# Optimization experiments

Measured on AMD Instinct MI355X. Metric: run time of the kernel, lower is better.

## Reference

```python
import jax, jax.numpy as jnp
import numpy as np

B = 2048
NUM_FIELDS = 32
EMBED = 64
P = NUM_FIELDS * (NUM_FIELDS - 1) // 2  # 496 field pairs

# Pair indices (i < j), identical to the row_idx/col_idx loops in __init__
_ROW, _COL = np.triu_indices(NUM_FIELDS, k=1)
ROW_IDX = jnp.asarray(_ROW, dtype=jnp.int32)
COL_IDX = jnp.asarray(_COL, dtype=jnp.int32)


def setup_inputs() -> dict:
    key = jax.random.key(0)
    k1, k2 = jax.random.split(key)
    emb_inputs = jax.random.normal(k1, (B, NUM_FIELDS, EMBED), dtype=jnp.float32)
    # kernel_type='mat' -> kernel shape (E, P, E), xavier_normal-like init
    fan_in = P * EMBED
    fan_out = EMBED
    std = float(np.sqrt(2.0 / (fan_in + fan_out)))
    kernel = jax.random.normal(k2, (EMBED, P, EMBED), dtype=jnp.float32) * std
    return {"emb_inputs": emb_inputs, "kernel": kernel}


def reference(emb_inputs, kernel):
    # Gather field pairs: p, q shape (B, P, E)
    p = emb_inputs[:, ROW_IDX]
    q = emb_inputs[:, COL_IDX]
    # torch named-tensor chain for kernel_type='mat':
    #   kp[b, h, n] = sum_e p[b, n, e] * kernel[h, n, e]
    #   out[b, n]   = sum_h kp[b, h, n] * q[b, n, h]
    # Fused: out[b, n] = sum_{e, h} p[b, n, e] * kernel[h, n, e] * q[b, n, h]
    return jnp.einsum('bne,hne,bnh->bn', p, kernel, q)
```

## Files before the change

### kernel.cpp

```cpp
#include <hip/hip_runtime.h>


#define B_TOT 2048
#define NF    32
#define EMB   64
#define NP    496
#define BT    32

typedef short bf16x8 __attribute__((ext_vector_type(8)));
typedef short bf16x4 __attribute__((ext_vector_type(4)));
typedef float f32x4  __attribute__((ext_vector_type(4)));

static __device__ inline unsigned f2bf(float f) {
    unsigned u = __builtin_bit_cast(unsigned, f);
    u += 0x7fffu + ((u >> 16) & 1u);
    return u >> 16;
}
static __device__ inline unsigned pack2(float lo, float hi) {
    return f2bf(lo) | (f2bf(hi) << 16);
}
static __device__ inline float bf2f(short s) {
    return __builtin_bit_cast(float, (unsigned)((unsigned short)s) << 16);
}

#define AS1 __attribute__((address_space(1)))
#define AS3 __attribute__((address_space(3)))

__device__ const unsigned char PAIR_T16[120] = {
    0x01,0x02,0x03,0x04,0x05,0x06,0x07,0x08,0x09,0x0A,0x0B,0x0C,0x0D,0x0E,0x0F,
    0x12,0x13,0x14,0x15,0x16,0x17,0x18,0x19,0x1A,0x1B,0x1C,0x1D,0x1E,0x1F,
    0x23,0x24,0x25,0x26,0x27,0x28,0x29,0x2A,0x2B,0x2C,0x2D,0x2E,0x2F,
    0x34,0x35,0x36,0x37,0x38,0x39,0x3A,0x3B,0x3C,0x3D,0x3E,0x3F,
    0x45,0x46,0x47,0x48,0x49,0x4A,0x4B,0x4C,0x4D,0x4E,0x4F,
    0x56,0x57,0x58,0x59,0x5A,0x5B,0x5C,0x5D,0x5E,0x5F,
    0x67,0x68,0x69,0x6A,0x6B,0x6C,0x6D,0x6E,0x6F,
    0x78,0x79,0x7A,0x7B,0x7C,0x7D,0x7E,0x7F,
    0x89,0x8A,0x8B,0x8C,0x8D,0x8E,0x8F,
    0x9A,0x9B,0x9C,0x9D,0x9E,0x9F,
    0xAB,0xAC,0xAD,0xAE,0xAF,
    0xBC,0xBD,0xBE,0xBF,
    0xCD,0xCE,0xCF,
    0xDE,0xDF,
    0xEF
};

__global__ __launch_bounds__(256) void prep(const float* __restrict__ kern,
                                            const float* __restrict__ emb,
                                            short* __restrict__ kb,
                                            short* __restrict__ ebf) {
    __shared__ short w[EMB * 72];
    if (blockIdx.x < NP) {
        const int n = blockIdx.x;
#pragma unroll
        for (int j = 0; j < 4; ++j) {
            const int idx = threadIdx.x + 256 * j;
            const int h = idx >> 4, e4 = idx & 15;
            const f32x4 v = *(const f32x4*)(kern + ((size_t)h * NP + n) * EMB + e4 * 4);
            uint2 u;
            u.x = pack2(v[0], v[1]);
            u.y = pack2(v[2], v[3]);
            *(uint2*)&w[h * 72 + e4 * 4] = u;
        }
        __syncthreads();
#pragma unroll
        for (int j = 0; j < 2; ++j) {
            const int u    = threadIdx.x + 256 * j;
            const int frag = u >> 6, l = u & 63;
            const int h  = (frag >> 1) * 16 + (l & 15);
            const int e0 = (frag & 1) * 32 + (l >> 4) * 8;
            const bf16x8 t = *(const bf16x8*)&w[h * 72 + e0];
            *(bf16x8*)(kb + (size_t)n * 4096 + u * 8) = t;
        }
    } else {
        const int t    = (blockIdx.x - NP) * 256 + threadIdx.x;
        const int cidx = t & 127;
        const int f    = (t >> 7) & 31;
        const int bt16 = t >> 12;
        const int bp = cidx >> 3, x = cidx & 7;
        const int ec = x ^ (bp & 7);
        const float* src = emb + (((size_t)(bt16 * 16 + bp) * NF + f) * EMB + ec * 8);
        const f32x4 a = *(const f32x4*)src;
        const f32x4 b = *(const f32x4*)(src + 4);
        uint4 u;
        u.x = pack2(a[0], a[1]); u.y = pack2(a[2], a[3]);
        u.z = pack2(b[0], b[1]); u.w = pack2(b[2], b[3]);
        *(uint4*)(ebf + (size_t)t * 8) = u;
    }
}

__global__ __launch_bounds__(512, 4) void opnl_main(
    const short* __restrict__ ebf,
    const short* __restrict__ kb,
    float* __restrict__ out)
{
    __shared__ short elds[16 * 2 * 1024];

    const int type = blockIdx.x >> 6;
    const int bt   = blockIdx.x & 63;
    const int b0   = bt * BT;

    int bLo, bHi, npr;
    switch (type) {
        case 0: case 1: bLo = 0;  bHi = 0;  npr = 60; break;
        case 2: case 3: bLo = 16; bHi = 16; npr = 60; break;
        case 4:         bLo = 0;  bHi = 8;  npr = 64; break;
        case 5:         bLo = 8;  bHi = 16; npr = 64; break;
        case 6:         bLo = 0;  bHi = 16; npr = 64; break;
        default:        bLo = 8;  bHi = 8;  npr = 64; break;
    }

    const int lane = threadIdx.x & 63;
    const int wid  = threadIdx.x >> 6;
    const int lo4  = lane & 15;
    const int hi4  = lane >> 4;

#pragma unroll
    for (int i = 0; i < 4; ++i) {
        const int s   = wid * 4 + i;
        const int lf  = s >> 1, sub = s & 1;
        const int gf  = lf + (lf < 8 ? bLo : bHi);
        const short* src = ebf + ((size_t)((bt * 2 + sub) * 32 + gf)) * 1024;
        __builtin_amdgcn_global_load_lds((const AS1 void*)(src + lane * 8),
                                         (AS3 void*)&elds[s * 1024], 16, 0, 0);
        __builtin_amdgcn_global_load_lds((const AS1 void*)(src + 512 + lane * 8),
                                         (AS3 void*)&elds[s * 1024 + 512], 16, 0, 0);
    }
    __syncthreads();

    auto pairK = [&](int k, int& lr, int& lc, int& nn) {
        int pr = wid + 8 * k;
        if (pr >= npr) pr -= npr;
        if (type < 4) {
            const int pig = __builtin_amdgcn_readfirstlane((type & 1) * 60 + pr);
            const int byt = PAIR_T16[pig];
            lr = byt >> 4; lc = byt & 15;
        } else {
            lr = pr >> 3; lc = 8 + (pr & 7);
        }
        const int R = lr + (lr < 8 ? bLo : bHi);
        const int C = lc + (lc < 8 ? bLo : bHi);
        nn = R * (63 - R) / 2 + (C - R - 1);
    };

    auto loadW = [&](bf16x8 (&wf)[4][2], int nn) {
        const bf16x8* wp = (const bf16x8*)(kb + (size_t)nn * 4096);
#pragma unroll
        for (int mh = 0; mh < 4; ++mh)
#pragma unroll
            for (int kc = 0; kc < 2; ++kc)
                wf[mh][kc] = wp[(mh * 2 + kc) * 64 + lane];
    };

    auto compute = [&](bf16x8 (&wf)[4][2], int lr, int lc, int nn) {
#pragma unroll
        for (int sub = 0; sub < 2; ++sub) {
            const int bb = sub * 16 + lo4;

            bf16x8 pf0 = *(const bf16x8*)
                &elds[(lr * 2 + sub) * 1024 + (lo4 * 8 + ((0 * 4 + hi4) ^ (lo4 & 7))) * 8];
            bf16x8 pf1 = *(const bf16x8*)
                &elds[(lr * 2 + sub) * 1024 + (lo4 * 8 + ((1 * 4 + hi4) ^ (lo4 & 7))) * 8];
            bf16x4 q0 = *(const bf16x4*)
                &elds[(lc * 2 + sub) * 1024 + (lo4 * 8 + ((0 + (hi4 >> 1)) ^ (lo4 & 7))) * 8 + (hi4 & 1) * 4];
            bf16x4 q1 = *(const bf16x4*)
                &elds[(lc * 2 + sub) * 1024 + (lo4 * 8 + ((2 + (hi4 >> 1)) ^ (lo4 & 7))) * 8 + (hi4 & 1) * 4];
            bf16x4 q2 = *(const bf16x4*)
                &elds[(lc * 2 + sub) * 1024 + (lo4 * 8 + ((4 + (hi4 >> 1)) ^ (lo4 & 7))) * 8 + (hi4 & 1) * 4];
            bf16x4 q3 = *(const bf16x4*)
                &elds[(lc * 2 + sub) * 1024 + (lo4 * 8 + ((6 + (hi4 >> 1)) ^ (lo4 & 7))) * 8 + (hi4 & 1) * 4];

            f32x4 acc[4] = {f32x4{0,0,0,0}, f32x4{0,0,0,0},
                            f32x4{0,0,0,0}, f32x4{0,0,0,0}};
            __builtin_amdgcn_s_setprio(1);
#pragma unroll
            for (int mh = 0; mh < 4; ++mh) {
                acc[mh] = __builtin_amdgcn_mfma_f32_16x16x32_bf16(
                    wf[mh][0], pf0, acc[mh], 0, 0, 0);
                acc[mh] = __builtin_amdgcn_mfma_f32_16x16x32_bf16(
                    wf[mh][1], pf1, acc[mh], 0, 0, 0);
            }
            __builtin_amdgcn_s_setprio(0);

            float v0 = acc[0][0] * bf2f(q0[0]);
            float v1 = acc[1][0] * bf2f(q1[0]);
            float v2 = acc[2][0] * bf2f(q2[0]);
            float v3 = acc[3][0] * bf2f(q3[0]);
            v0 = fmaf(acc[0][1], bf2f(q0[1]), v0);
            v1 = fmaf(acc[1][1], bf2f(q1[1]), v1);
            v2 = fmaf(acc[2][1], bf2f(q2[1]), v2);
            v3 = fmaf(acc[3][1], bf2f(q3[1]), v3);
            v0 = fmaf(acc[0][2], bf2f(q0[2]), v0);
            v1 = fmaf(acc[1][2], bf2f(q1[2]), v1);
            v2 = fmaf(acc[2][2], bf2f(q2[2]), v2);
            v3 = fmaf(acc[3][2], bf2f(q3[2]), v3);
            v0 = fmaf(acc[0][3], bf2f(q0[3]), v0);
            v1 = fmaf(acc[1][3], bf2f(q1[3]), v1);
            v2 = fmaf(acc[2][3], bf2f(q2[3]), v2);
            v3 = fmaf(acc[3][3], bf2f(q3[3]), v3);
            float val = (v0 + v1) + (v2 + v3);

            val += __shfl_xor(val, 16, 64);
            val += __shfl_xor(val, 32, 64);
            if (lane < 16) out[(size_t)(b0 + bb) * NP + nn] = val;
        }
    };

    bf16x8 wA[4][2], wB[4][2];
    int lrA, lcA, nA, lrB, lcB, nB;
    pairK(0, lrA, lcA, nA);
    loadW(wA, nA);
#pragma unroll
    for (int k = 0; k < 8; ++k) {
        if ((k & 1) == 0) {
            if (k < 7) { pairK(k + 1, lrB, lcB, nB); loadW(wB, nB); }
            compute(wA, lrA, lcA, nA);
        } else {
            if (k < 7) { pairK(k + 1, lrA, lcA, nA); loadW(wA, nA); }
            compute(wB, lrB, lcB, nB);
        }
    }
}

extern "C" void kernel_launch(void* const* d_in, const int* in_sizes, int n_in,
                              void* d_out, int out_size, void* d_ws, size_t ws_size,
                              hipStream_t stream) {
    const float* emb  = (const float*)d_in[0];
    const float* kern = (const float*)d_in[1];
    float*       out  = (float*)d_out;

    short* kb  = (short*)d_ws;
    short* ebf = (short*)((char*)d_ws + (4 << 20));

    prep<<<NP + (B_TOT * NF * EMB / 8) / 256, 256, 0, stream>>>(kern, emb, kb, ebf);
    opnl_main<<<8 * 64, 512, 0, stream>>>(ebf, kb, out);
}
```

Measured before the change: 29.68 us.

## Give each wave a contiguous pair range and cache row operand fragments

Block index mapping is changed so the eight pair-types of one batch tile are adjacent in launch order, which may improve L2 sharing of embedding tiles. Each wave now processes a contiguous slice of pairs instead of a strided one, so consecutive pairs often share the same row field. The row (p) fragments are then kept in registers and reloaded from LDS only when the row changes. The cost is extra registers for the cached fragments and a runtime branch on the row index, which could raise register pressure or hurt scheduling under the unrolled loop.

```diff
diff --git a/kernel.cpp b/kernel.cpp
--- a/kernel.cpp
+++ b/kernel.cpp
@@ -95,8 +95,8 @@
 {
     __shared__ short elds[16 * 2 * 1024];
 
-    const int type = blockIdx.x >> 6;
-    const int bt   = blockIdx.x & 63;
+    const int type = blockIdx.x & 7;
+    const int bt   = blockIdx.x >> 3;
     const int b0   = bt * BT;
 
     int bLo, bHi, npr;
@@ -127,9 +127,12 @@
     }
     __syncthreads();
 
+    const int s_ = (wid * npr) >> 3;
+    const int e_ = ((wid + 1) * npr) >> 3;
+
     auto pairK = [&](int k, int& lr, int& lc, int& nn) {
-        int pr = wid + 8 * k;
-        if (pr >= npr) pr -= npr;
+        int pr = s_ + k;
+        if (pr >= e_) pr = s_;
         if (type < 4) {
             const int pig = __builtin_amdgcn_readfirstlane((type & 1) * 60 + pr);
             const int byt = PAIR_T16[pig];
@@ -151,15 +154,25 @@
                 wf[mh][kc] = wp[(mh * 2 + kc) * 64 + lane];
     };
 
-    auto compute = [&](bf16x8 (&wf)[4][2], int lr, int lc, int nn) {
+    bf16x8 pfc[2][2];
+    int lr_prev = -1;
+    auto loadP = [&](int lr) {
+        if (lr == lr_prev) return;
+        lr_prev = lr;
+#pragma unroll
+        for (int sub = 0; sub < 2; ++sub)
+#pragma unroll
+            for (int kc = 0; kc < 2; ++kc)
+                pfc[sub][kc] = *(const bf16x8*)
+                    &elds[(lr * 2 + sub) * 1024 +
+                          (lo4 * 8 + ((kc * 4 + hi4) ^ (lo4 & 7))) * 8];
+    };
+
+    auto compute = [&](bf16x8 (&wf)[4][2], int lc, int nn) {
 #pragma unroll
         for (int sub = 0; sub < 2; ++sub) {
             const int bb = sub * 16 + lo4;
 
-            bf16x8 pf0 = *(const bf16x8*)
-                &elds[(lr * 2 + sub) * 1024 + (lo4 * 8 + ((0 * 4 + hi4) ^ (lo4 & 7))) * 8];
-            bf16x8 pf1 = *(const bf16x8*)
-                &elds[(lr * 2 + sub) * 1024 + (lo4 * 8 + ((1 * 4 + hi4) ^ (lo4 & 7))) * 8];
             bf16x4 q0 = *(const bf16x4*)
                 &elds[(lc * 2 + sub) * 1024 + (lo4 * 8 + ((0 + (hi4 >> 1)) ^ (lo4 & 7))) * 8 + (hi4 & 1) * 4];
             bf16x4 q1 = *(const bf16x4*)
@@ -175,9 +188,9 @@
 #pragma unroll
             for (int mh = 0; mh < 4; ++mh) {
                 acc[mh] = __builtin_amdgcn_mfma_f32_16x16x32_bf16(
-                    wf[mh][0], pf0, acc[mh], 0, 0, 0);
+                    wf[mh][0], pfc[sub][0], acc[mh], 0, 0, 0);
                 acc[mh] = __builtin_amdgcn_mfma_f32_16x16x32_bf16(
-                    wf[mh][1], pf1, acc[mh], 0, 0, 0);
+                    wf[mh][1], pfc[sub][1], acc[mh], 0, 0, 0);
             }
             __builtin_amdgcn_s_setprio(0);
 
@@ -213,10 +226,10 @@
     for (int k = 0; k < 8; ++k) {
         if ((k & 1) == 0) {
             if (k < 7) { pairK(k + 1, lrB, lcB, nB); loadW(wB, nB); }
-            compute(wA, lrA, lcA, nA);
+            loadP(lrA); compute(wA, lcA, nA);
         } else {
             if (k < 7) { pairK(k + 1, lrA, lcA, nA); loadW(wA, nA); }
-            compute(wB, lrB, lcB, nB);
+            loadP(lrB); compute(wB, lcB, nB);
         }
     }
 }
```

New measurement: 39.30 us. 32.4% more time.
